# Performance work log

Hardware: AMD Instinct MI355X
Metric: run time of the kernel (lower is better)

The kernel has to match this reference:

```python
import jax, jax.numpy as jnp
import numpy as np

IN_FEATURES = 4096
OUT_FEATURES = 11008
BATCH, SEQ = 8, 16


def setup_inputs() -> dict:
    key = jax.random.key(0)
    k_in, k_w, k_s, k_b = jax.random.split(key, 4)
    inp = jax.random.normal(k_in, (BATCH, SEQ, IN_FEATURES), dtype=jnp.float32)
    # int8 weights in [-128, 127], as torch.randint(-128, 127, ...)
    quantized_weights = jax.random.randint(
        k_w, (OUT_FEATURES, IN_FEATURES), -128, 127, dtype=jnp.int32
    ).astype(jnp.int8)
    scales = jax.random.normal(k_s, (OUT_FEATURES,), dtype=jnp.float32)
    bias = jax.random.normal(k_b, (1, OUT_FEATURES), dtype=jnp.float32)
    return {"input": inp, "quantized_weights": quantized_weights,
            "scales": scales, "bias": bias}


def reference(input, quantized_weights, scales, bias):
    # dequantize weight to activation dtype, then linear: y = x @ W^T
    w = quantized_weights.astype(input.dtype)  # [O, I]
    out = jnp.einsum("bsi,oi->bso", input, w)  # [B, S, O]
    out = out * scales  # per-output-channel scale
    out = out + bias    # bias shape [1, O] broadcasts
    return out
```

## Files before the change

### kernel.cpp

```cpp
#include <hip/hip_runtime.h>
#include <stdint.h>


#define M_ROWS 128
#define K_DIM  4096
#define N_DIM  11008
#define CHUNKS 64
#define NT64   (N_DIM / 64)
#define XP_BYTES (M_ROWS * K_DIM * 2)
#define PART_ELEMS ((size_t)M_ROWS * (size_t)N_DIM)

typedef __attribute__((ext_vector_type(8))) short bf16x8;
typedef __attribute__((ext_vector_type(4))) float f32x4;
typedef const unsigned __attribute__((address_space(1)))* gas1_t;
typedef unsigned __attribute__((address_space(3)))* las3_t;

__device__ __forceinline__ unsigned bf16_rn(float f) {
  unsigned u = __float_as_uint(f);
  return (u + 0x7FFFu + ((u >> 16) & 1u)) >> 16;
}
__device__ __forceinline__ unsigned pk2(int a, int b) {
  unsigned lo = __float_as_uint((float)a), hi = __float_as_uint((float)b);
#if __has_builtin(__builtin_amdgcn_perm)
  return __builtin_amdgcn_perm(hi, lo, 0x07060302u);
#else
  return (hi & 0xFFFF0000u) | (lo >> 16);
#endif
}

__device__ __forceinline__ void gload_lds16(const void* g, void* lds) {
#if __has_builtin(__builtin_amdgcn_global_load_lds)
  __builtin_amdgcn_global_load_lds((gas1_t)g, (las3_t)(size_t)(unsigned)(size_t)lds,
                                   16, 0, 0);
#else
  *(uint4*)lds = *(const uint4*)g;
#endif
}

__global__ __launch_bounds__(256) void pack_x_kernel(
    const float* __restrict__ x, unsigned short* __restrict__ xp) {
  int tid  = blockIdx.x * 256 + threadIdx.x;
  int lane = tid & 63;
  int h    = (tid >> 6) & 1;
  int mf   = (tid >> 7) & 7;
  int kk   = tid >> 10;
  int m     = mf * 16 + (lane & 15);
  int kbase = kk * 64 + h * 32 + ((lane >> 4) * 8);
  const float* src = x + (size_t)m * K_DIM + kbase;
  float4 f0 = *(const float4*)(src);
  float4 f1 = *(const float4*)(src + 4);
  float v[8] = {f0.x, f0.y, f0.z, f0.w, f1.x, f1.y, f1.z, f1.w};
  unsigned po[4];
#pragma unroll
  for (int i = 0; i < 4; ++i)
    po[i] = bf16_rn(v[2 * i]) | (bf16_rn(v[2 * i + 1]) << 16);
  *(uint4*)(xp + (size_t)tid * 8) = *(uint4*)po;
}

struct BReg { uint4 v[4]; };

__global__ __launch_bounds__(256, 3) void gemm4w_kernel(
    const unsigned short* __restrict__ xp,
    const int* __restrict__ wq,
    const float* __restrict__ scales,
    const float* __restrict__ bias,
    float* __restrict__ dst,
    int ks) {
  __shared__ char As0[16384];
  __shared__ char As1[16384];

  const int tid  = threadIdx.x;
  const int lane = tid & 63;
  const int w    = tid >> 6;
  const int nt   = blockIdx.x;
  const int kz   = blockIdx.y;
  const int cpb  = CHUNKS / ks;
  const int kk0  = kz * cpb;
  const size_t n0 = (size_t)nt * 64 + (size_t)w * 16;
  const int l15 = lane & 15, lh = lane >> 4;

  const char* agp = (const char*)xp + (size_t)kk0 * 16384 + tid * 16;
  const int* bptr = wq + (n0 + (size_t)l15) * K_DIM + (size_t)kk0 * 64 + lh * 8;

  f32x4 acc[8];
  {
    f32x4 z = {0.f, 0.f, 0.f, 0.f};
#pragma unroll
    for (int i = 0; i < 8; ++i) acc[i] = z;
  }

  auto STAGE = [&](int t, char* buf) {
#pragma unroll
    for (int i = 0; i < 4; ++i)
      gload_lds16(agp + (size_t)t * 16384 + (size_t)i * 4096,
                  buf + tid * 16 + i * 4096);
  };
  auto LOADB = [&](int t, BReg& R) {
    const int* bp = bptr + t * 64;
    R.v[0] = *(const uint4*)(bp);
    R.v[1] = *(const uint4*)(bp + 4);
    R.v[2] = *(const uint4*)(bp + 32);
    R.v[3] = *(const uint4*)(bp + 36);
  };
  auto COMP = [&](const char* ab, BReg& R) {
    bf16x8 cv[2];
#pragma unroll
    for (int s = 0; s < 2; ++s) {
      union { unsigned u[4]; bf16x8 b; } c;
      c.u[0] = pk2((int)R.v[s * 2].x,     (int)R.v[s * 2].y);
      c.u[1] = pk2((int)R.v[s * 2].z,     (int)R.v[s * 2].w);
      c.u[2] = pk2((int)R.v[s * 2 + 1].x, (int)R.v[s * 2 + 1].y);
      c.u[3] = pk2((int)R.v[s * 2 + 1].z, (int)R.v[s * 2 + 1].w);
      cv[s] = c.b;
    }
#pragma unroll
    for (int mf = 0; mf < 8; ++mf)
#pragma unroll
      for (int s = 0; s < 2; ++s) {
        bf16x8 a = *(const bf16x8*)(ab + (mf * 2 + s) * 1024 + lane * 16);
        acc[mf] = __builtin_amdgcn_mfma_f32_16x16x32_bf16(a, cv[s], acc[mf], 0, 0, 0);
      }
  };

  BReg R0, R1;
  STAGE(0, As0);
  LOADB(0, R0);
  __syncthreads();

#pragma unroll 1
  for (int tt = 0; tt < cpb; tt += 2) {
    STAGE(tt + 1, As1);
    LOADB(tt + 1, R1);
    COMP(As0, R0);
    __syncthreads();
    if (tt + 2 < cpb) { STAGE(tt + 2, As0); LOADB(tt + 2, R0); }
    COMP(As1, R1);
    __syncthreads();
  }

  if (ks == 1) {
    const size_t n = n0 + (size_t)l15;
    const float sc = scales[n], bi = bias[n];
#pragma unroll
    for (int mf = 0; mf < 8; ++mf) {
      const int mb = mf * 16 + lh * 4;
#pragma unroll
      for (int r = 0; r < 4; ++r)
        dst[(size_t)(mb + r) * N_DIM + n] = sc * acc[mf][r] + bi;
    }
  } else {
    float* pb = dst + (size_t)kz * PART_ELEMS + n0 + l15;
#pragma unroll
    for (int mf = 0; mf < 8; ++mf) {
      const int mb = mf * 16 + lh * 4;
#pragma unroll
      for (int r = 0; r < 4; ++r)
        pb[(size_t)(mb + r) * N_DIM] = acc[mf][r];
    }
  }
}

__global__ __launch_bounds__(256) void reduce_kernel(
    const float* __restrict__ part, const float* __restrict__ scales,
    const float* __restrict__ bias, float* __restrict__ out, int ks) {
  const int m = blockIdx.y;
  const int c4 = blockIdx.x * 256 + threadIdx.x;
  if (c4 >= N_DIM / 4) return;
  const size_t n = (size_t)c4 * 4;
  const float* p = part + (size_t)m * N_DIM + n;
  float4 s = *(const float4*)(p);
  for (int z = 1; z < ks; ++z) {
    float4 q = *(const float4*)(p + (size_t)z * PART_ELEMS);
    s.x += q.x; s.y += q.y; s.z += q.z; s.w += q.w;
  }
  float4 sc = *(const float4*)(scales + n);
  float4 bi = *(const float4*)(bias + n);
  float4 r;
  r.x = sc.x * s.x + bi.x;
  r.y = sc.y * s.y + bi.y;
  r.z = sc.z * s.z + bi.z;
  r.w = sc.w * s.w + bi.w;
  *(float4*)(out + (size_t)m * N_DIM + n) = r;
}

__global__ __launch_bounds__(256) void naive_kernel(
    const float* __restrict__ x, const int* __restrict__ wq,
    const float* __restrict__ scales, const float* __restrict__ bias,
    float* __restrict__ out) {
  const int n = blockIdx.x * 256 + threadIdx.x;
  const int m = blockIdx.y;
  const float* xr = x + (size_t)m * K_DIM;
  const int* wr = wq + (size_t)n * K_DIM;
  float s = 0.f;
  for (int k = 0; k < K_DIM; k += 4) {
    float4 xv = *(const float4*)(xr + k);
    int4  wv = *(const int4*)(wr + k);
    s += xv.x * (float)wv.x + xv.y * (float)wv.y +
         xv.z * (float)wv.z + xv.w * (float)wv.w;
  }
  out[(size_t)m * N_DIM + n] = scales[n] * s + bias[n];
}

extern "C" void kernel_launch(void* const* d_in, const int* in_sizes, int n_in,
                              void* d_out, int out_size, void* d_ws, size_t ws_size,
                              hipStream_t stream) {
  const float* x      = (const float*)d_in[0];
  const int* wq       = (const int*)d_in[1];
  const float* scales = (const float*)d_in[2];
  const float* bias   = (const float*)d_in[3];
  float* out          = (float*)d_out;

  const size_t need4 = (size_t)XP_BYTES + 4 * PART_ELEMS * sizeof(float);
  const size_t need2 = (size_t)XP_BYTES + 2 * PART_ELEMS * sizeof(float);
  int ks = (ws_size >= need4) ? 4 : (ws_size >= need2) ? 2
         : (ws_size >= (size_t)XP_BYTES) ? 1 : 0;
  if (ks == 0) {
    naive_kernel<<<dim3(N_DIM / 256, M_ROWS), 256, 0, stream>>>(x, wq, scales, bias, out);
    return;
  }
  unsigned short* xp = (unsigned short*)d_ws;
  float* part        = (float*)((char*)d_ws + XP_BYTES);

  pack_x_kernel<<<256, 256, 0, stream>>>(x, xp);
  gemm4w_kernel<<<dim3(NT64, ks), 256, 0, stream>>>(
      xp, wq, scales, bias, ks == 1 ? out : part, ks);
  if (ks > 1)
    reduce_kernel<<<dim3((N_DIM / 4 + 255) / 256, M_ROWS), 256, 0, stream>>>(
        part, scales, bias, out, ks);
}
```

Baseline: 54.41 us.

## Drop split-K reduction and use a 4-stage LDS pipeline with counted waits

Removes the split-K path, so the partial-sum buffers and the separate reduce kernel are gone. Each of the 172 blocks now walks the whole K dimension. A 4-buffer LDS ring plus register prefetch two chunks ahead replaces the double buffer, with raw s_waitcnt vmcnt and s_barrier so loads stay in flight across barriers. The aim is to cut the partial-sum traffic and the extra launch. The cost is a grid of only 172 blocks on a GPU with many more CUs, so parallelism per block is lower and the occupancy hint falls to 1.

```diff
diff --git a/kernel.cpp b/kernel.cpp
--- a/kernel.cpp
+++ b/kernel.cpp
@@ -8,7 +8,6 @@
 #define CHUNKS 64
 #define NT64   (N_DIM / 64)
 #define XP_BYTES (M_ROWS * K_DIM * 2)
-#define PART_ELEMS ((size_t)M_ROWS * (size_t)N_DIM)
 
 typedef __attribute__((ext_vector_type(8))) short bf16x8;
 typedef __attribute__((ext_vector_type(4))) float f32x4;
@@ -37,6 +36,11 @@
 #endif
 }
 
+#define BAR()    asm volatile("s_barrier" ::: "memory")
+#define WBAR16() asm volatile("s_waitcnt vmcnt(16)\n\ts_barrier" ::: "memory")
+#define WBAR8()  asm volatile("s_waitcnt vmcnt(8)\n\ts_barrier" ::: "memory")
+#define WBAR0()  asm volatile("s_waitcnt vmcnt(0)\n\ts_barrier" ::: "memory")
+
 __global__ __launch_bounds__(256) void pack_x_kernel(
     const float* __restrict__ x, unsigned short* __restrict__ xp) {
   int tid  = blockIdx.x * 256 + threadIdx.x;
@@ -59,28 +63,23 @@
 
 struct BReg { uint4 v[4]; };
 
-__global__ __launch_bounds__(256, 3) void gemm4w_kernel(
+__global__ __launch_bounds__(256, 1) void gemm4w_kernel(
     const unsigned short* __restrict__ xp,
     const int* __restrict__ wq,
     const float* __restrict__ scales,
     const float* __restrict__ bias,
-    float* __restrict__ dst,
-    int ks) {
-  __shared__ char As0[16384];
-  __shared__ char As1[16384];
+    float* __restrict__ out) {
+  __shared__ char As[4 * 16384];
 
   const int tid  = threadIdx.x;
   const int lane = tid & 63;
   const int w    = tid >> 6;
   const int nt   = blockIdx.x;
-  const int kz   = blockIdx.y;
-  const int cpb  = CHUNKS / ks;
-  const int kk0  = kz * cpb;
   const size_t n0 = (size_t)nt * 64 + (size_t)w * 16;
   const int l15 = lane & 15, lh = lane >> 4;
 
-  const char* agp = (const char*)xp + (size_t)kk0 * 16384 + tid * 16;
-  const int* bptr = wq + (n0 + (size_t)l15) * K_DIM + (size_t)kk0 * 64 + lh * 8;
+  const char* agp = (const char*)xp + tid * 16;
+  const int* bptr = wq + (n0 + (size_t)l15) * K_DIM + lh * 8;
 
   f32x4 acc[8];
   {
@@ -89,11 +88,11 @@
     for (int i = 0; i < 8; ++i) acc[i] = z;
   }
 
-  auto STAGE = [&](int t, char* buf) {
+  auto STAGE = [&](int t, int bufOff) {
 #pragma unroll
     for (int i = 0; i < 4; ++i)
       gload_lds16(agp + (size_t)t * 16384 + (size_t)i * 4096,
-                  buf + tid * 16 + i * 4096);
+                  As + bufOff + tid * 16 + i * 4096);
   };
   auto LOADB = [&](int t, BReg& R) {
     const int* bp = bptr + t * 64;
@@ -122,65 +121,43 @@
       }
   };
 
-  BReg R0, R1;
-  STAGE(0, As0);
+#define PHASE(T, RCUR, RNXT)                       \
+    LOADB((T) + 2, RNXT);                          \
+    BAR();                                         \
+    STAGE((T) + 2, (((T) + 2) & 3) * 16384);       \
+    WBAR16();                                      \
+    COMP(As + ((T) & 3) * 16384, RCUR);
+
+  BReg R0, R1, R2, R3;
+  STAGE(0, 0);
   LOADB(0, R0);
-  __syncthreads();
+  STAGE(1, 16384);
+  LOADB(1, R1);
 
 #pragma unroll 1
-  for (int tt = 0; tt < cpb; tt += 2) {
-    STAGE(tt + 1, As1);
-    LOADB(tt + 1, R1);
-    COMP(As0, R0);
-    __syncthreads();
-    if (tt + 2 < cpb) { STAGE(tt + 2, As0); LOADB(tt + 2, R0); }
-    COMP(As1, R1);
-    __syncthreads();
+  for (int t = 0; t < CHUNKS - 4; t += 4) {
+    PHASE(t + 0, R0, R2);
+    PHASE(t + 1, R1, R3);
+    PHASE(t + 2, R2, R0);
+    PHASE(t + 3, R3, R1);
   }
+  PHASE(CHUNKS - 4, R0, R2);
+  PHASE(CHUNKS - 3, R1, R3);
+  WBAR8();
+  COMP(As + 2 * 16384, R2);
+  WBAR0();
+  COMP(As + 3 * 16384, R3);
+#undef PHASE
 
-  if (ks == 1) {
-    const size_t n = n0 + (size_t)l15;
-    const float sc = scales[n], bi = bias[n];
+  const size_t n = n0 + (size_t)l15;
+  const float sc = scales[n], bi = bias[n];
 #pragma unroll
-    for (int mf = 0; mf < 8; ++mf) {
-      const int mb = mf * 16 + lh * 4;
+  for (int mf = 0; mf < 8; ++mf) {
+    const int mb = mf * 16 + lh * 4;
 #pragma unroll
-      for (int r = 0; r < 4; ++r)
-        dst[(size_t)(mb + r) * N_DIM + n] = sc * acc[mf][r] + bi;
-    }
-  } else {
-    float* pb = dst + (size_t)kz * PART_ELEMS + n0 + l15;
-#pragma unroll
-    for (int mf = 0; mf < 8; ++mf) {
-      const int mb = mf * 16 + lh * 4;
-#pragma unroll
-      for (int r = 0; r < 4; ++r)
-        pb[(size_t)(mb + r) * N_DIM] = acc[mf][r];
-    }
+    for (int r = 0; r < 4; ++r)
+      out[(size_t)(mb + r) * N_DIM + n] = sc * acc[mf][r] + bi;
   }
-}
-
-__global__ __launch_bounds__(256) void reduce_kernel(
-    const float* __restrict__ part, const float* __restrict__ scales,
-    const float* __restrict__ bias, float* __restrict__ out, int ks) {
-  const int m = blockIdx.y;
-  const int c4 = blockIdx.x * 256 + threadIdx.x;
-  if (c4 >= N_DIM / 4) return;
-  const size_t n = (size_t)c4 * 4;
-  const float* p = part + (size_t)m * N_DIM + n;
-  float4 s = *(const float4*)(p);
-  for (int z = 1; z < ks; ++z) {
-    float4 q = *(const float4*)(p + (size_t)z * PART_ELEMS);
-    s.x += q.x; s.y += q.y; s.z += q.z; s.w += q.w;
-  }
-  float4 sc = *(const float4*)(scales + n);
-  float4 bi = *(const float4*)(bias + n);
-  float4 r;
-  r.x = sc.x * s.x + bi.x;
-  r.y = sc.y * s.y + bi.y;
-  r.z = sc.z * s.z + bi.z;
-  r.w = sc.w * s.w + bi.w;
-  *(float4*)(out + (size_t)m * N_DIM + n) = r;
 }
 
 __global__ __launch_bounds__(256) void naive_kernel(
@@ -210,21 +187,12 @@
   const float* bias   = (const float*)d_in[3];
   float* out          = (float*)d_out;
 
-  const size_t need4 = (size_t)XP_BYTES + 4 * PART_ELEMS * sizeof(float);
-  const size_t need2 = (size_t)XP_BYTES + 2 * PART_ELEMS * sizeof(float);
-  int ks = (ws_size >= need4) ? 4 : (ws_size >= need2) ? 2
-         : (ws_size >= (size_t)XP_BYTES) ? 1 : 0;
-  if (ks == 0) {
+  if (ws_size < (size_t)XP_BYTES) {
     naive_kernel<<<dim3(N_DIM / 256, M_ROWS), 256, 0, stream>>>(x, wq, scales, bias, out);
     return;
   }
   unsigned short* xp = (unsigned short*)d_ws;
-  float* part        = (float*)((char*)d_ws + XP_BYTES);
 
   pack_x_kernel<<<256, 256, 0, stream>>>(x, xp);
-  gemm4w_kernel<<<dim3(NT64, ks), 256, 0, stream>>>(
-      xp, wq, scales, bias, ks == 1 ? out : part, ks);
-  if (ks > 1)
-    reduce_kernel<<<dim3((N_DIM / 4 + 255) / 256, M_ROWS), 256, 0, stream>>>(
-        part, scales, bias, out, ks);
+  gemm4w_kernel<<<dim3(NT64), 256, 0, stream>>>(xp, wq, scales, bias, out);
 }
```

New measurement: 64.32 us. +18.2%, slower.
